# Kernel optimization log

Hardware: AMD Instinct MI355X
Metric: run time of the kernel (lower is better)

Reference implementation:

```python
import jax, jax.numpy as jnp
import numpy as np

D_MODEL = 512
NUM_HEADS = 8
D_FF = 2048
SEQ = 2048
BATCH = 2
EPS = 1e-5


def _linear(x, W, b):
    # x: [S,B,D_in], W: [D_out, D_in] (torch convention), b: [D_out]
    return jnp.einsum('sbd,ed->sbe', x, W) + b


def _layer_norm(x, g, b):
    mu = jnp.mean(x, axis=-1, keepdims=True)
    var = jnp.var(x, axis=-1, keepdims=True)
    return (x - mu) * jax.lax.rsqrt(var + EPS) * g + b


def _mha(q_in, k_in, v_in, W, b, mask4d, num_heads):
    # q_in: [Sq,B,D], k_in/v_in: [Sk,B,D]; W: [4,D,D], b: [4,D]
    Sq, B, D = q_in.shape
    Sk = k_in.shape[0]
    dk = D // num_heads
    q = _linear(q_in, W[0], b[0]).reshape(Sq, B, num_heads, dk).transpose(1, 2, 0, 3)
    k = _linear(k_in, W[1], b[1]).reshape(Sk, B, num_heads, dk).transpose(1, 2, 0, 3)
    v = _linear(v_in, W[2], b[2]).reshape(Sk, B, num_heads, dk).transpose(1, 2, 0, 3)
    scores = jnp.einsum('bhqd,bhkd->bhqk', q, k) / jnp.sqrt(jnp.asarray(dk, q.dtype))
    scores = jnp.where(mask4d, -jnp.inf, scores)
    p = jax.nn.softmax(scores, axis=-1)  # dropout p=0 -> identity
    o = jnp.einsum('bhqk,bhkd->bhqd', p, v)  # [B,H,Sq,dk]
    o = o.transpose(2, 0, 1, 3).reshape(Sq, B, D)
    return _linear(o, W[3], b[3])


def setup_inputs() -> dict:
    key = jax.random.key(0)
    ks = jax.random.split(key, 12)
    scale = 1.0 / np.sqrt(D_MODEL)
    inp = {
        'x': jax.random.normal(ks[0], (SEQ, BATCH, D_MODEL), jnp.float32),
        'memory': jax.random.normal(ks[1], (SEQ, BATCH, D_MODEL), jnp.float32),
        # causal mask: True = masked (strictly upper triangular)
        'tgt_mask': jnp.triu(jnp.ones((SEQ, SEQ), dtype=bool), k=1),
        # per-batch key padding mask for cross attention
        'memory_mask': jax.random.randint(ks[2], (BATCH, SEQ), 0, 2) > 0,
        'sa_W': jax.random.normal(ks[3], (4, D_MODEL, D_MODEL), jnp.float32) * scale,
        'sa_b': jnp.zeros((4, D_MODEL), jnp.float32),
        'ca_W': jax.random.normal(ks[4], (4, D_MODEL, D_MODEL), jnp.float32) * scale,
        'ca_b': jnp.zeros((4, D_MODEL), jnp.float32),
        'w1': jax.random.normal(ks[5], (D_FF, D_MODEL), jnp.float32) * scale,
        'b1': jnp.zeros((D_FF,), jnp.float32),
        'w2': jax.random.normal(ks[6], (D_MODEL, D_FF), jnp.float32) * (1.0 / np.sqrt(D_FF)),
        'b2': jnp.zeros((D_MODEL,), jnp.float32),
        'ln_g': jnp.ones((3, D_MODEL), jnp.float32),
        'ln_b': jnp.zeros((3, D_MODEL), jnp.float32),
    }
    return inp


def reference(x, memory, tgt_mask, memory_mask, sa_W, sa_b, ca_W, ca_b,
              w1, b1, w2, b2, ln_g, ln_b):
    # self-attention block (pre-norm, residual)
    nx = _layer_norm(x, ln_g[0], ln_b[0])
    sa = _mha(nx, nx, nx, sa_W, sa_b, tgt_mask[None, None], NUM_HEADS)
    x = x + sa
    # cross-attention block
    nx = _layer_norm(x, ln_g[1], ln_b[1])
    ca = _mha(nx, memory, memory, ca_W, ca_b, memory_mask[:, None, None, :], NUM_HEADS)
    x = x + ca
    # FFN block
    nx = _layer_norm(x, ln_g[2], ln_b[2])
    ff = _linear(jax.nn.relu(_linear(nx, w1, b1)), w2, b2)
    return x + ff
```

## Files before the change

### kernel.cpp

```cpp
#include <hip/hip_runtime.h>

#define S_LEN 2048
#define BATCH_N 2
#define DM 512
#define H_N 8
#define DK_N 64
#define FF_N 2048
#define M_TOK (S_LEN*BATCH_N)
#define QSZ (BATCH_N*H_N*S_LEN*DK_N)

typedef __attribute__((ext_vector_type(8))) short short8;
typedef __attribute__((ext_vector_type(4))) float f32x4;
typedef __attribute__((ext_vector_type(16))) float f32x16;
typedef __attribute__((ext_vector_type(4))) unsigned uint4v;

__device__ __forceinline__ unsigned short f2b(float f) {
  union { float f; unsigned u; } v; v.f = f;
  unsigned r = v.u + 0x7FFFu + ((v.u >> 16) & 1u);
  return (unsigned short)(r >> 16);
}
__device__ __forceinline__ float b2f(unsigned short u) {
  union { unsigned u; float f; } v; v.u = ((unsigned)u) << 16; return v.f;
}

__device__ __forceinline__ void gl_lds16(const void* g, void* l) {
  __builtin_amdgcn_global_load_lds(
      (__attribute__((address_space(1))) unsigned int*)(unsigned long long)g,
      (__attribute__((address_space(3))) unsigned int*)(unsigned int)(unsigned long long)l,
      16, 0, 0);
}

__global__ void cast_kernel(const float* __restrict__ src,
                            unsigned short* __restrict__ dst, int n) {
  int i = (blockIdx.x * blockDim.x + threadIdx.x) * 4;
  if (i >= n) return;
  float4 v = *(const float4*)(src + i);
  ushort4 o; o.x = f2b(v.x); o.y = f2b(v.y); o.z = f2b(v.z); o.w = f2b(v.w);
  *(ushort4*)(dst + i) = o;
}

__global__ void maskpack(const int* __restrict__ mm, unsigned long long* __restrict__ bm) {
  int t = threadIdx.x;
  int b = t >> 5, kt = t & 31;
  unsigned long long m = 0ull;
  for (int j = 0; j < 64; j++)
    m |= (unsigned long long)(mm[b*S_LEN + kt*64 + j] != 0) << j;
  bm[b*32 + kt] = m;
}

__global__ __launch_bounds__(128) void ln_kernel(const float* __restrict__ in,
                                                 const float* __restrict__ g,
                                                 const float* __restrict__ b,
                                                 unsigned short* __restrict__ out) {
  int row = blockIdx.x, t = threadIdx.x;
  float4 v = ((const float4*)(in + (size_t)row * DM))[t];
  float s  = v.x + v.y + v.z + v.w;
  float ss = v.x*v.x + v.y*v.y + v.z*v.z + v.w*v.w;
  #pragma unroll
  for (int off = 32; off >= 1; off >>= 1) {
    s  += __shfl_xor(s,  off);
    ss += __shfl_xor(ss, off);
  }
  __shared__ float sh[4];
  if ((t & 63) == 0) { sh[(t>>6)*2] = s; sh[(t>>6)*2+1] = ss; }
  __syncthreads();
  s = sh[0] + sh[2]; ss = sh[1] + sh[3];
  float mean = s * (1.f/512.f);
  float inv  = rsqrtf(ss * (1.f/512.f) - mean*mean + 1e-5f);
  float4 gv = ((const float4*)g)[t];
  float4 bv = ((const float4*)b)[t];
  ushort4 o;
  o.x = f2b((v.x-mean)*inv*gv.x + bv.x);
  o.y = f2b((v.y-mean)*inv*gv.y + bv.y);
  o.z = f2b((v.z-mean)*inv*gv.z + bv.z);
  o.w = f2b((v.w-mean)*inv*gv.w + bv.w);
  ((ushort4*)out)[(size_t)row*128 + t] = o;
}

template<int RELU, int OUTMODE, int RESID>
__global__ __launch_bounds__(256) void gemm_bt(
    const unsigned short* __restrict__ A, const unsigned short* __restrict__ W,
    const float* __restrict__ bias, const float* __restrict__ resid,
    float* __restrict__ Cf, unsigned short* __restrict__ Cb,
    int M, int N, int K)
{
  __shared__ unsigned short As[64*40];
  __shared__ unsigned short Bs[64*40];
  int tid = threadIdx.x;
  int lane = tid & 63, w = tid >> 6;
  int wr = w >> 1, wc = w & 1;
  int bm = blockIdx.y * 64, bn = blockIdx.x * 64;
  f32x4 acc[2][2] = {};
  int lrow = tid >> 2;
  int lcg  = (tid & 3) * 8;
  const size_t aoff = (size_t)(bm + lrow) * K + lcg;
  const size_t boff = (size_t)(bn + lrow) * K + lcg;
  int fr = lane & 15, kg = (lane >> 4) * 8;
  short8 pa = *(const short8*)&A[aoff];
  short8 pb = *(const short8*)&W[boff];
  for (int k0 = 0; k0 < K; k0 += 32) {
    *(short8*)&As[lrow*40 + lcg] = pa;
    *(short8*)&Bs[lrow*40 + lcg] = pb;
    if (k0 + 32 < K) {
      pa = *(const short8*)&A[aoff + k0 + 32];
      pb = *(const short8*)&W[boff + k0 + 32];
    }
    __syncthreads();
    short8 af0 = *(const short8*)&As[(wr*32 +      fr)*40 + kg];
    short8 af1 = *(const short8*)&As[(wr*32 + 16 + fr)*40 + kg];
    short8 bf0 = *(const short8*)&Bs[(wc*32 +      fr)*40 + kg];
    short8 bf1 = *(const short8*)&Bs[(wc*32 + 16 + fr)*40 + kg];
    acc[0][0] = __builtin_amdgcn_mfma_f32_16x16x32_bf16(af0, bf0, acc[0][0], 0,0,0);
    acc[0][1] = __builtin_amdgcn_mfma_f32_16x16x32_bf16(af0, bf1, acc[0][1], 0,0,0);
    acc[1][0] = __builtin_amdgcn_mfma_f32_16x16x32_bf16(af1, bf0, acc[1][0], 0,0,0);
    acc[1][1] = __builtin_amdgcn_mfma_f32_16x16x32_bf16(af1, bf1, acc[1][1], 0,0,0);
    __syncthreads();
  }
  int rbase = (lane >> 4) * 4;
  #pragma unroll
  for (int m = 0; m < 2; m++) {
    #pragma unroll
    for (int n = 0; n < 2; n++) {
      int col = bn + wc*32 + n*16 + (lane & 15);
      float bc = bias[col];
      #pragma unroll
      for (int r = 0; r < 4; r++) {
        int row = bm + wr*32 + m*16 + rbase + r;
        float vv = acc[m][n][r] + bc;
        if (RELU) vv = fmaxf(vv, 0.f);
        if (OUTMODE == 2) {
          int which = col >> 9, hh = (col >> 6) & 7, dd = col & 63;
          size_t idx = ((((size_t)which*BATCH_N + (row & 1))*H_N + hh)*S_LEN + (row >> 1))*DK_N + dd;
          Cb[idx] = f2b(vv);
        } else {
          size_t idx = (size_t)row * N + col;
          if (RESID) vv += resid[idx];
          if (OUTMODE == 1) Cb[idx] = f2b(vv);
          else              Cf[idx] = vv;
        }
      }
    }
  }
}

template<int RELU, int OUTMODE, int VSTART>
__global__ __launch_bounds__(256) void gemm128(
    const unsigned short* __restrict__ A, const unsigned short* __restrict__ W,
    const float* __restrict__ bias, unsigned short* __restrict__ Cb,
    int M, int N, int K)
{
  __shared__ unsigned short As[128*32];
  __shared__ unsigned short Bs[128*32];
  int tid = threadIdx.x, lane = tid & 63, w = tid >> 6;
  int bm = blockIdx.y * 128, bn = blockIdx.x * 128;
  int fr = lane & 15, hi = lane >> 4;
  int kg8 = hi*8, rg = hi*4;
  int wm = (w >> 1) * 64, wn = (w & 1) * 64;
  f32x4 acc[4][4] = {};
  const unsigned short* ga0 = A + (size_t)(bm +      (tid>>2))*K + (tid&3)*8;
  const unsigned short* ga1 = A + (size_t)(bm + 64 + (tid>>2))*K + (tid&3)*8;
  const unsigned short* gb0 = W + (size_t)(bn +      (tid>>2))*K + (tid&3)*8;
  const unsigned short* gb1 = W + (size_t)(bn + 64 + (tid>>2))*K + (tid&3)*8;
  unsigned short* lA0 = &As[tid*8];
  unsigned short* lA1 = &As[2048 + tid*8];
  unsigned short* lB0 = &Bs[tid*8];
  unsigned short* lB1 = &Bs[2048 + tid*8];
  for (int k0 = 0; k0 < K; k0 += 32) {
    gl_lds16(ga0 + k0, lA0);
    gl_lds16(ga1 + k0, lA1);
    gl_lds16(gb0 + k0, lB0);
    gl_lds16(gb1 + k0, lB1);
    __syncthreads();
    short8 af[4], bf[4];
    #pragma unroll
    for (int m = 0; m < 4; m++) af[m] = *(const short8*)&As[(wm + m*16 + fr)*32 + kg8];
    #pragma unroll
    for (int n = 0; n < 4; n++) bf[n] = *(const short8*)&Bs[(wn + n*16 + fr)*32 + kg8];
    __builtin_amdgcn_s_setprio(1);
    #pragma unroll
    for (int m = 0; m < 4; m++)
      #pragma unroll
      for (int n = 0; n < 4; n++)
        acc[m][n] = __builtin_amdgcn_mfma_f32_16x16x32_bf16(af[m], bf[n], acc[m][n], 0,0,0);
    __builtin_amdgcn_s_setprio(0);
    __syncthreads();
  }
  #pragma unroll
  for (int m = 0; m < 4; m++) {
    #pragma unroll
    for (int n = 0; n < 4; n++) {
      int col = bn + wn + n*16 + fr;
      float bc = bias[col];
      #pragma unroll
      for (int r = 0; r < 4; r++) {
        int row = bm + wm + m*16 + rg + r;
        float vv = acc[m][n][r] + bc;
        if (RELU) vv = fmaxf(vv, 0.f);
        if (OUTMODE == 2) {
          int which = col >> 9, hh = (col >> 6) & 7, dd = col & 63;
          int srow = row >> 1, bb = row & 1;
          size_t idx;
          if (which >= VSTART)
            idx = (size_t)which*QSZ + (((size_t)bb*H_N + hh)*DK_N + dd)*S_LEN + srow;
          else
            idx = (size_t)which*QSZ + (((size_t)bb*H_N + hh)*S_LEN + srow)*DK_N + dd;
          Cb[idx] = f2b(vv);
        } else {
          Cb[(size_t)row * N + col] = f2b(vv);
        }
      }
    }
  }
}

template<int MODE>
__global__ __launch_bounds__(256, 4) void attn2(
    const unsigned short* __restrict__ qg, const unsigned short* __restrict__ kpl,
    const unsigned short* __restrict__ vtpl, const unsigned long long* __restrict__ bm,
    unsigned short* __restrict__ opart, float* __restrict__ lpart)
{
  __shared__ unsigned short SM[2*64*72 + 128];
  unsigned short* Ks = SM;
  unsigned short* Vt = SM + 64*72;
  float* lsum = (float*)(SM + 2*64*72);
  int tid = threadIdx.x;
  int lane = tid & 63, w = tid >> 6;
  int qgp = w & 1, kh2 = w >> 1;
  int l31 = lane & 31, hi5 = lane >> 5;
  int bid = blockIdx.x;
  int p = bid & 15, u = bid >> 4;
  int qt = u >> 2, range = u & 3;
  int h = p & 7, b = p >> 3;
  const size_t sbase = (size_t)(b*H_N + h) * S_LEN;
  int kt0 = range*8, kt1 = kt0 + 7;
  if (MODE == 0) {
    if (kt0 > qt) {
      int zr = tid >> 2, zc = (tid & 3) * 16;
      short8 z = {};
      size_t zb = (size_t)range*QSZ + (sbase + (size_t)qt*64 + zr)*DK_N + zc;
      *(short8*)&opart[zb]     = z;
      *(short8*)&opart[zb + 8] = z;
      if (tid < 64) lpart[range*32768 + (int)sbase + qt*64 + tid] = 0.f;
      return;
    }
    if (kt1 > qt) kt1 = qt;
  }
  int qrow = qt*64 + qgp*32 + l31;
  short8 qf[4];
  #pragma unroll
  for (int km = 0; km < 4; km++)
    qf[km] = *(const short8*)&qg[(sbase + qrow)*DK_N + km*16 + hi5*8];

  f32x16 oa0 = {}, oa1 = {};
  float lp = 0.f;
  for (int kt = kt0; kt <= kt1; kt++) {
    __syncthreads();
    {
      int sr = tid >> 2, sc = (tid & 3) * 16;
      const unsigned short* kg = &kpl[(sbase + (size_t)kt*64 + sr)*DK_N + sc];
      *(short8*)&Ks[sr*72 + sc]     = *(const short8*)kg;
      *(short8*)&Ks[sr*72 + sc + 8] = *(const short8*)(kg + 8);
      const unsigned short* vg = &vtpl[((size_t)(b*H_N + h)*DK_N + sr)*S_LEN + kt*64 + sc];
      *(short8*)&Vt[sr*72 + sc]     = *(const short8*)vg;
      *(short8*)&Vt[sr*72 + sc + 8] = *(const short8*)(vg + 8);
    }
    __syncthreads();
    f32x16 sa = {};
    __builtin_amdgcn_s_setprio(1);
    #pragma unroll
    for (int km = 0; km < 4; km++) {
      short8 kf = *(const short8*)&Ks[(kh2*32 + l31)*72 + km*16 + hi5*8];
      sa = __builtin_amdgcn_mfma_f32_32x32x16_bf16(kf, qf[km], sa, 0, 0, 0);
    }
    __builtin_amdgcn_s_setprio(0);
    unsigned mlo = 0;
    if (MODE == 1) {
      unsigned long long mw = bm[b*32 + kt];
      mlo = (unsigned)(mw >> (kh2*32 + 4*hi5));
    }
    float pv[16];
    float psum = 0.f;
    int qv = qgp*32 + l31;
    #pragma unroll
    for (int r = 0; r < 16; r++) {
      const int pos = (r & 3) + 8*(r >> 2);
      float e = __expf(sa[r] * 0.125f);
      bool dead;
      if (MODE == 0) dead = (kt == qt) && (kh2*32 + 4*hi5 + pos > qv);
      else           dead = ((mlo >> pos) & 1u) != 0u;
      e = dead ? 0.f : e;
      pv[r] = e;
      psum += e;
    }
    lp += psum;
    unsigned pk[8];
    #pragma unroll
    for (int i = 0; i < 8; i++)
      asm("v_cvt_pk_bf16_f32 %0, %1, %2" : "=v"(pk[i]) : "v"(pv[2*i]), "v"(pv[2*i+1]));
    asm("v_permlane32_swap_b32 %0, %1" : "+v"(pk[0]), "+v"(pk[2]));
    asm("v_permlane32_swap_b32 %0, %1" : "+v"(pk[1]), "+v"(pk[3]));
    asm("v_permlane32_swap_b32 %0, %1" : "+v"(pk[4]), "+v"(pk[6]));
    asm("v_permlane32_swap_b32 %0, %1" : "+v"(pk[5]), "+v"(pk[7]));
    uint4v f0v, f1v;
    f0v.x = pk[0]; f0v.y = pk[1]; f0v.z = pk[2]; f0v.w = pk[3];
    f1v.x = pk[4]; f1v.y = pk[5]; f1v.z = pk[6]; f1v.w = pk[7];
    short8 pf0 = *(short8*)&f0v;
    short8 pf1 = *(short8*)&f1v;
    __builtin_amdgcn_s_setprio(1);
    {
      short8 v00 = *(const short8*)&Vt[(     l31)*72 + kh2*32 +      hi5*8];
      short8 v01 = *(const short8*)&Vt[(     l31)*72 + kh2*32 + 16 + hi5*8];
      oa0 = __builtin_amdgcn_mfma_f32_32x32x16_bf16(pf0, v00, oa0, 0, 0, 0);
      oa0 = __builtin_amdgcn_mfma_f32_32x32x16_bf16(pf1, v01, oa0, 0, 0, 0);
      short8 v10 = *(const short8*)&Vt[(32 + l31)*72 + kh2*32 +      hi5*8];
      short8 v11 = *(const short8*)&Vt[(32 + l31)*72 + kh2*32 + 16 + hi5*8];
      oa1 = __builtin_amdgcn_mfma_f32_32x32x16_bf16(pf0, v10, oa1, 0, 0, 0);
      oa1 = __builtin_amdgcn_mfma_f32_32x32x16_bf16(pf1, v11, oa1, 0, 0, 0);
    }
    __builtin_amdgcn_s_setprio(0);
  }
  float lptot = lp + __shfl_xor(lp, 32);
  float* fb = (float*)SM;
  __syncthreads();
  if (kh2 == 1) {
    #pragma unroll
    for (int r = 0; r < 16; r++) {
      const int pos = (r & 3) + 8*(r >> 2);
      int qr = qgp*32 + pos + 4*hi5;
      fb[qr*64 + l31]      = oa0[r];
      fb[qr*64 + 32 + l31] = oa1[r];
    }
    if (lane < 32) lsum[qgp*32 + l31] = lptot;
  }
  __syncthreads();
  if (kh2 == 0) {
    if (lane < 32)
      lpart[range*32768 + (int)sbase + qt*64 + qgp*32 + l31] = lptot + lsum[qgp*32 + l31];
    #pragma unroll
    for (int r = 0; r < 16; r++) {
      const int pos = (r & 3) + 8*(r >> 2);
      int qr = qgp*32 + pos + 4*hi5;
      size_t obase = (size_t)range*QSZ + (sbase + (size_t)qt*64 + qr)*DK_N;
      opart[obase + l31]      = f2b(oa0[r] + fb[qr*64 + l31]);
      opart[obase + 32 + l31] = f2b(oa1[r] + fb[qr*64 + 32 + l31]);
    }
  }
}

__global__ __launch_bounds__(256) void attn_combine4(
    const unsigned short* __restrict__ op, const float* __restrict__ lp,
    unsigned short* __restrict__ o)
{
  int t = blockIdx.x*256 + threadIdx.x;
  int f = t*8;
  int col = f & 511, row = f >> 9;
  int h = col >> 6, d = col & 63, s = row >> 1, b = row & 1;
  size_t pr = ((size_t)b*H_N + h)*S_LEN + s;
  size_t base = pr*DK_N + d;
  float acc[8] = {0.f,0.f,0.f,0.f,0.f,0.f,0.f,0.f};
  float l = 0.f;
  #pragma unroll
  for (int r = 0; r < 4; r++) {
    short8 a = *(const short8*)&op[(size_t)r*QSZ + base];
    #pragma unroll
    for (int i = 0; i < 8; i++) acc[i] += b2f((unsigned short)a[i]);
    l += lp[r*32768 + (int)pr];
  }
  float inv = 1.f / l;
  short8 r8;
  #pragma unroll
  for (int i = 0; i < 8; i++) r8[i] = (short)f2b(acc[i] * inv);
  *(short8*)&o[(size_t)row*DM + col] = r8;
}

extern "C" void kernel_launch(void* const* d_in, const int* in_sizes, int n_in,
                              void* d_out, int out_size, void* d_ws, size_t ws_size,
                              hipStream_t stream) {
  const float* x       = (const float*)d_in[0];
  const float* memory  = (const float*)d_in[1];
  const int*   memmask = (const int*)d_in[3];
  const float* sa_W = (const float*)d_in[4];
  const float* sa_b = (const float*)d_in[5];
  const float* ca_W = (const float*)d_in[6];
  const float* ca_b = (const float*)d_in[7];
  const float* w1   = (const float*)d_in[8];
  const float* b1   = (const float*)d_in[9];
  const float* w2   = (const float*)d_in[10];
  const float* b2   = (const float*)d_in[11];
  const float* ln_g = (const float*)d_in[12];
  const float* ln_b = (const float*)d_in[13];
  float* out = (float*)d_out;

  char* ws = (char*)d_ws;
  float*          xcur   = (float*)ws;
  unsigned short* nx_bf  = (unsigned short*)(ws + (8u<<20));
  unsigned short* qkv_sa = (unsigned short*)(ws + (12u<<20));
  unsigned short* q_ca   = (unsigned short*)(ws + (24u<<20));
  unsigned short* kv_ca  = (unsigned short*)(ws + (28u<<20));
  unsigned short* o_bf   = (unsigned short*)(ws + (36u<<20));
  unsigned short* mem_bf = (unsigned short*)(ws + (40u<<20));
  unsigned short* h_bf   = (unsigned short*)(ws + (44u<<20));
  unsigned short* opart  = (unsigned short*)(ws + (44u<<20));
  float*          lpart  = (float*)(ws + (60u<<20));
  unsigned long long* bmsk = (unsigned long long*)(ws + (60u<<20) + (1u<<19));
  unsigned short* w_sa   = (unsigned short*)(ws + (61u<<20));
  unsigned short* w_ca   = w_sa + 4*512*512;
  unsigned short* w_f1   = w_ca + 4*512*512;
  unsigned short* w_f2   = w_f1 + 2048*512;

  cast_kernel<<<1024, 256, 0, stream>>>(sa_W, w_sa, 4*512*512);
  cast_kernel<<<1024, 256, 0, stream>>>(ca_W, w_ca, 4*512*512);
  cast_kernel<<<1024, 256, 0, stream>>>(w1,   w_f1, 2048*512);
  cast_kernel<<<1024, 256, 0, stream>>>(w2,   w_f2, 512*2048);
  cast_kernel<<<2048, 256, 0, stream>>>(memory, mem_bf, M_TOK*512);
  maskpack<<<1, 64, 0, stream>>>(memmask, bmsk);

  dim3 blk(256);
  dim3 g512 (512/64,  4096/64);
  dim3 q128_1536(1536/128, 4096/128);
  dim3 q128_1024(1024/128, 4096/128);
  dim3 q128_2048(2048/128, 4096/128);

  ln_kernel<<<4096, 128, 0, stream>>>(x, ln_g, ln_b, nx_bf);
  gemm128<0,2,2><<<q128_1536, blk, 0, stream>>>(nx_bf, w_sa, sa_b, qkv_sa, 4096, 1536, 512);
  attn2<0><<<2048, 256, 0, stream>>>(qkv_sa, qkv_sa + QSZ, qkv_sa + 2*QSZ, nullptr, opart, lpart);
  attn_combine4<<<1024, 256, 0, stream>>>(opart, lpart, o_bf);
  gemm_bt<0,0,1><<<g512, blk, 0, stream>>>(o_bf, w_sa + 3*262144, sa_b + 1536, x, xcur, nullptr, 4096, 512, 512);

  ln_kernel<<<4096, 128, 0, stream>>>(xcur, ln_g + 512, ln_b + 512, nx_bf);
  gemm_bt<0,2,0><<<g512, blk, 0, stream>>>(nx_bf, w_ca, ca_b, nullptr, nullptr, q_ca, 4096, 512, 512);
  gemm128<0,2,1><<<q128_1024, blk, 0, stream>>>(mem_bf, w_ca + 262144, ca_b + 512, kv_ca, 4096, 1024, 512);
  attn2<1><<<2048, 256, 0, stream>>>(q_ca, kv_ca, kv_ca + QSZ, bmsk, opart, lpart);
  attn_combine4<<<1024, 256, 0, stream>>>(opart, lpart, o_bf);
  gemm_bt<0,0,1><<<g512, blk, 0, stream>>>(o_bf, w_ca + 3*262144, ca_b + 1536, xcur, xcur, nullptr, 4096, 512, 512);

  ln_kernel<<<4096, 128, 0, stream>>>(xcur, ln_g + 1024, ln_b + 1024, nx_bf);
  gemm128<1,1,0><<<q128_2048, blk, 0, stream>>>(nx_bf, w_f1, b1, h_bf, 4096, 2048, 512);
  gemm_bt<0,0,1><<<g512, blk, 0, stream>>>(h_bf, w_f2, b2, xcur, out, nullptr, 4096, 512, 2048);
}
```

Measured before the change: 212.3 us.

## Use 128-row query tiles in attention, double-buffer GEMM LDS, merge prep casts

The attention kernel now gives each wave its own 32 query rows over all 64 keys of a tile, with 128-query tiles per block. This halves the grid and drops the cross-wave LDS reduction of partial outputs, so each K/V tile loaded is reused by twice as many queries. The 64x64 GEMM gets double-buffered shared memory, which removes one barrier per k-step and overlaps the next tile's LDS store with the MFMAs. The six weight/memory cast and mask-pack launches are fused into a single prep kernel to cut launch overhead. In exchange, the attention kernel has a lower occupancy hint, fewer blocks and more causal imbalance per block.

```diff
diff --git a/kernel.cpp b/kernel.cpp
--- a/kernel.cpp
+++ b/kernel.cpp
@@ -30,22 +30,34 @@
       16, 0, 0);
 }
 
-__global__ void cast_kernel(const float* __restrict__ src,
-                            unsigned short* __restrict__ dst, int n) {
-  int i = (blockIdx.x * blockDim.x + threadIdx.x) * 4;
-  if (i >= n) return;
+__device__ __forceinline__ void cast4(const float* __restrict__ src,
+                                      unsigned short* __restrict__ dst, int i) {
   float4 v = *(const float4*)(src + i);
   ushort4 o; o.x = f2b(v.x); o.y = f2b(v.y); o.z = f2b(v.z); o.w = f2b(v.w);
   *(ushort4*)(dst + i) = o;
 }
 
-__global__ void maskpack(const int* __restrict__ mm, unsigned long long* __restrict__ bm) {
-  int t = threadIdx.x;
-  int b = t >> 5, kt = t & 31;
-  unsigned long long m = 0ull;
-  for (int j = 0; j < 64; j++)
-    m |= (unsigned long long)(mm[b*S_LEN + kt*64 + j] != 0) << j;
-  bm[b*32 + kt] = m;
+__global__ __launch_bounds__(256) void prep_kernel(
+    const float* __restrict__ sa_W, const float* __restrict__ ca_W,
+    const float* __restrict__ w1, const float* __restrict__ w2,
+    const float* __restrict__ memory, const int* __restrict__ mm,
+    unsigned short* __restrict__ o_sa, unsigned short* __restrict__ o_ca,
+    unsigned short* __restrict__ o_w1, unsigned short* __restrict__ o_w2,
+    unsigned short* __restrict__ o_mem, unsigned long long* __restrict__ bmo)
+{
+  int blk = blockIdx.x, t = threadIdx.x;
+  if (blk < 1024)      cast4(sa_W, o_sa, (blk*256 + t)*4);
+  else if (blk < 2048) cast4(ca_W, o_ca, ((blk-1024)*256 + t)*4);
+  else if (blk < 3072) cast4(w1,   o_w1, ((blk-2048)*256 + t)*4);
+  else if (blk < 4096) cast4(w2,   o_w2, ((blk-3072)*256 + t)*4);
+  else if (blk < 6144) cast4(memory, o_mem, ((blk-4096)*256 + t)*4);
+  else if (t < 64) {
+    int b = t >> 5, kt = t & 31;
+    unsigned long long m = 0ull;
+    for (int j = 0; j < 64; j++)
+      m |= (unsigned long long)(mm[b*S_LEN + kt*64 + j] != 0) << j;
+    bmo[b*32 + kt] = m;
+  }
 }
 
 __global__ __launch_bounds__(128) void ln_kernel(const float* __restrict__ in,
@@ -84,8 +96,8 @@
     float* __restrict__ Cf, unsigned short* __restrict__ Cb,
     int M, int N, int K)
 {
-  __shared__ unsigned short As[64*40];
-  __shared__ unsigned short Bs[64*40];
+  __shared__ unsigned short As[2][64*40];
+  __shared__ unsigned short Bs[2][64*40];
   int tid = threadIdx.x;
   int lane = tid & 63, w = tid >> 6;
   int wr = w >> 1, wc = w & 1;
@@ -98,23 +110,30 @@
   int fr = lane & 15, kg = (lane >> 4) * 8;
   short8 pa = *(const short8*)&A[aoff];
   short8 pb = *(const short8*)&W[boff];
+  *(short8*)&As[0][lrow*40 + lcg] = pa;
+  *(short8*)&Bs[0][lrow*40 + lcg] = pb;
+  __syncthreads();
+  int cur = 0;
   for (int k0 = 0; k0 < K; k0 += 32) {
-    *(short8*)&As[lrow*40 + lcg] = pa;
-    *(short8*)&Bs[lrow*40 + lcg] = pb;
-    if (k0 + 32 < K) {
+    bool hn = (k0 + 32) < K;
+    if (hn) {
       pa = *(const short8*)&A[aoff + k0 + 32];
       pb = *(const short8*)&W[boff + k0 + 32];
     }
-    __syncthreads();
-    short8 af0 = *(const short8*)&As[(wr*32 +      fr)*40 + kg];
-    short8 af1 = *(const short8*)&As[(wr*32 + 16 + fr)*40 + kg];
-    short8 bf0 = *(const short8*)&Bs[(wc*32 +      fr)*40 + kg];
-    short8 bf1 = *(const short8*)&Bs[(wc*32 + 16 + fr)*40 + kg];
+    short8 af0 = *(const short8*)&As[cur][(wr*32 +      fr)*40 + kg];
+    short8 af1 = *(const short8*)&As[cur][(wr*32 + 16 + fr)*40 + kg];
+    short8 bf0 = *(const short8*)&Bs[cur][(wc*32 +      fr)*40 + kg];
+    short8 bf1 = *(const short8*)&Bs[cur][(wc*32 + 16 + fr)*40 + kg];
     acc[0][0] = __builtin_amdgcn_mfma_f32_16x16x32_bf16(af0, bf0, acc[0][0], 0,0,0);
     acc[0][1] = __builtin_amdgcn_mfma_f32_16x16x32_bf16(af0, bf1, acc[0][1], 0,0,0);
     acc[1][0] = __builtin_amdgcn_mfma_f32_16x16x32_bf16(af1, bf0, acc[1][0], 0,0,0);
     acc[1][1] = __builtin_amdgcn_mfma_f32_16x16x32_bf16(af1, bf1, acc[1][1], 0,0,0);
+    if (hn) {
+      *(short8*)&As[cur^1][lrow*40 + lcg] = pa;
+      *(short8*)&Bs[cur^1][lrow*40 + lcg] = pb;
+    }
     __syncthreads();
+    cur ^= 1;
   }
   int rbase = (lane >> 4) * 4;
   #pragma unroll
@@ -214,136 +233,124 @@
 }
 
 template<int MODE>
-__global__ __launch_bounds__(256, 4) void attn2(
+__global__ __launch_bounds__(256, 3) void attn3(
     const unsigned short* __restrict__ qg, const unsigned short* __restrict__ kpl,
     const unsigned short* __restrict__ vtpl, const unsigned long long* __restrict__ bm,
     unsigned short* __restrict__ opart, float* __restrict__ lpart)
 {
-  __shared__ unsigned short SM[2*64*72 + 128];
+  __shared__ unsigned short SM[2*64*72];
   unsigned short* Ks = SM;
   unsigned short* Vt = SM + 64*72;
-  float* lsum = (float*)(SM + 2*64*72);
   int tid = threadIdx.x;
   int lane = tid & 63, w = tid >> 6;
-  int qgp = w & 1, kh2 = w >> 1;
   int l31 = lane & 31, hi5 = lane >> 5;
   int bid = blockIdx.x;
   int p = bid & 15, u = bid >> 4;
-  int qt = u >> 2, range = u & 3;
+  int qtile = u >> 2, range = u & 3;
   int h = p & 7, b = p >> 3;
   const size_t sbase = (size_t)(b*H_N + h) * S_LEN;
   int kt0 = range*8, kt1 = kt0 + 7;
   if (MODE == 0) {
-    if (kt0 > qt) {
-      int zr = tid >> 2, zc = (tid & 3) * 16;
+    int ktmax_tile = qtile*2 + 1;
+    if (kt0 > ktmax_tile) {
+      int zr = tid >> 1, zc = (tid & 1) * 32;
       short8 z = {};
-      size_t zb = (size_t)range*QSZ + (sbase + (size_t)qt*64 + zr)*DK_N + zc;
-      *(short8*)&opart[zb]     = z;
-      *(short8*)&opart[zb + 8] = z;
-      if (tid < 64) lpart[range*32768 + (int)sbase + qt*64 + tid] = 0.f;
+      size_t zb = (size_t)range*QSZ + (sbase + (size_t)qtile*128 + zr)*DK_N + zc;
+      *(short8*)&opart[zb]      = z;
+      *(short8*)&opart[zb + 8]  = z;
+      *(short8*)&opart[zb + 16] = z;
+      *(short8*)&opart[zb + 24] = z;
+      if (tid < 128) lpart[range*32768 + (int)sbase + qtile*128 + tid] = 0.f;
       return;
     }
-    if (kt1 > qt) kt1 = qt;
-  }
-  int qrow = qt*64 + qgp*32 + l31;
+    if (kt1 > ktmax_tile) kt1 = ktmax_tile;
+  }
+  int qrow = qtile*128 + w*32 + l31;
   short8 qf[4];
   #pragma unroll
   for (int km = 0; km < 4; km++)
     qf[km] = *(const short8*)&qg[(sbase + qrow)*DK_N + km*16 + hi5*8];
+
+  int sr = tid >> 2, sc = (tid & 3) * 16;
+  const unsigned short* kbase = &kpl[(sbase + sr)*DK_N + sc];
+  const unsigned short* vbase = &vtpl[((size_t)(b*H_N + h)*DK_N + sr)*S_LEN + sc];
 
   f32x16 oa0 = {}, oa1 = {};
   float lp = 0.f;
   for (int kt = kt0; kt <= kt1; kt++) {
     __syncthreads();
     {
-      int sr = tid >> 2, sc = (tid & 3) * 16;
-      const unsigned short* kg = &kpl[(sbase + (size_t)kt*64 + sr)*DK_N + sc];
+      const unsigned short* kg = kbase + (size_t)kt*64*DK_N;
+      const unsigned short* vg = vbase + kt*64;
       *(short8*)&Ks[sr*72 + sc]     = *(const short8*)kg;
       *(short8*)&Ks[sr*72 + sc + 8] = *(const short8*)(kg + 8);
-      const unsigned short* vg = &vtpl[((size_t)(b*H_N + h)*DK_N + sr)*S_LEN + kt*64 + sc];
       *(short8*)&Vt[sr*72 + sc]     = *(const short8*)vg;
       *(short8*)&Vt[sr*72 + sc + 8] = *(const short8*)(vg + 8);
     }
     __syncthreads();
-    f32x16 sa = {};
-    __builtin_amdgcn_s_setprio(1);
-    #pragma unroll
-    for (int km = 0; km < 4; km++) {
-      short8 kf = *(const short8*)&Ks[(kh2*32 + l31)*72 + km*16 + hi5*8];
-      sa = __builtin_amdgcn_mfma_f32_32x32x16_bf16(kf, qf[km], sa, 0, 0, 0);
-    }
-    __builtin_amdgcn_s_setprio(0);
-    unsigned mlo = 0;
-    if (MODE == 1) {
-      unsigned long long mw = bm[b*32 + kt];
-      mlo = (unsigned)(mw >> (kh2*32 + 4*hi5));
-    }
-    float pv[16];
-    float psum = 0.f;
-    int qv = qgp*32 + l31;
-    #pragma unroll
-    for (int r = 0; r < 16; r++) {
-      const int pos = (r & 3) + 8*(r >> 2);
-      float e = __expf(sa[r] * 0.125f);
-      bool dead;
-      if (MODE == 0) dead = (kt == qt) && (kh2*32 + 4*hi5 + pos > qv);
-      else           dead = ((mlo >> pos) & 1u) != 0u;
-      e = dead ? 0.f : e;
-      pv[r] = e;
-      psum += e;
-    }
-    lp += psum;
-    unsigned pk[8];
-    #pragma unroll
-    for (int i = 0; i < 8; i++)
-      asm("v_cvt_pk_bf16_f32 %0, %1, %2" : "=v"(pk[i]) : "v"(pv[2*i]), "v"(pv[2*i+1]));
-    asm("v_permlane32_swap_b32 %0, %1" : "+v"(pk[0]), "+v"(pk[2]));
-    asm("v_permlane32_swap_b32 %0, %1" : "+v"(pk[1]), "+v"(pk[3]));
-    asm("v_permlane32_swap_b32 %0, %1" : "+v"(pk[4]), "+v"(pk[6]));
-    asm("v_permlane32_swap_b32 %0, %1" : "+v"(pk[5]), "+v"(pk[7]));
-    uint4v f0v, f1v;
-    f0v.x = pk[0]; f0v.y = pk[1]; f0v.z = pk[2]; f0v.w = pk[3];
-    f1v.x = pk[4]; f1v.y = pk[5]; f1v.z = pk[6]; f1v.w = pk[7];
-    short8 pf0 = *(short8*)&f0v;
-    short8 pf1 = *(short8*)&f1v;
-    __builtin_amdgcn_s_setprio(1);
-    {
-      short8 v00 = *(const short8*)&Vt[(     l31)*72 + kh2*32 +      hi5*8];
-      short8 v01 = *(const short8*)&Vt[(     l31)*72 + kh2*32 + 16 + hi5*8];
-      oa0 = __builtin_amdgcn_mfma_f32_32x32x16_bf16(pf0, v00, oa0, 0, 0, 0);
-      oa0 = __builtin_amdgcn_mfma_f32_32x32x16_bf16(pf1, v01, oa0, 0, 0, 0);
-      short8 v10 = *(const short8*)&Vt[(32 + l31)*72 + kh2*32 +      hi5*8];
-      short8 v11 = *(const short8*)&Vt[(32 + l31)*72 + kh2*32 + 16 + hi5*8];
-      oa1 = __builtin_amdgcn_mfma_f32_32x32x16_bf16(pf0, v10, oa1, 0, 0, 0);
-      oa1 = __builtin_amdgcn_mfma_f32_32x32x16_bf16(pf1, v11, oa1, 0, 0, 0);
-    }
-    __builtin_amdgcn_s_setprio(0);
+    #pragma unroll
+    for (int kb = 0; kb < 2; kb++) {
+      f32x16 sa = {};
+      __builtin_amdgcn_s_setprio(1);
+      #pragma unroll
+      for (int km = 0; km < 4; km++) {
+        short8 kf = *(const short8*)&Ks[(kb*32 + l31)*72 + km*16 + hi5*8];
+        sa = __builtin_amdgcn_mfma_f32_32x32x16_bf16(kf, qf[km], sa, 0, 0, 0);
+      }
+      __builtin_amdgcn_s_setprio(0);
+      unsigned mlo = 0;
+      if (MODE == 1) mlo = (unsigned)(bm[b*32 + kt] >> (kb*32 + 4*hi5));
+      float pv[16];
+      float psum = 0.f;
+      #pragma unroll
+      for (int r = 0; r < 16; r++) {
+        const int pos = (r & 3) + 8*(r >> 2);
+        float e = __expf(sa[r] * 0.125f);
+        bool dead;
+        if (MODE == 0) dead = (kt*64 + kb*32 + 4*hi5 + pos) > qrow;
+        else           dead = ((mlo >> pos) & 1u) != 0u;
+        e = dead ? 0.f : e;
+        pv[r] = e;
+        psum += e;
+      }
+      lp += psum;
+      unsigned pk[8];
+      #pragma unroll
+      for (int i = 0; i < 8; i++)
+        asm("v_cvt_pk_bf16_f32 %0, %1, %2" : "=v"(pk[i]) : "v"(pv[2*i]), "v"(pv[2*i+1]));
+      asm("v_permlane32_swap_b32 %0, %1" : "+v"(pk[0]), "+v"(pk[2]));
+      asm("v_permlane32_swap_b32 %0, %1" : "+v"(pk[1]), "+v"(pk[3]));
+      asm("v_permlane32_swap_b32 %0, %1" : "+v"(pk[4]), "+v"(pk[6]));
+      asm("v_permlane32_swap_b32 %0, %1" : "+v"(pk[5]), "+v"(pk[7]));
+      uint4v f0v, f1v;
+      f0v.x = pk[0]; f0v.y = pk[1]; f0v.z = pk[2]; f0v.w = pk[3];
+      f1v.x = pk[4]; f1v.y = pk[5]; f1v.z = pk[6]; f1v.w = pk[7];
+      short8 pf0 = *(short8*)&f0v;
+      short8 pf1 = *(short8*)&f1v;
+      __builtin_amdgcn_s_setprio(1);
+      {
+        short8 v00 = *(const short8*)&Vt[(     l31)*72 + kb*32 +      hi5*8];
+        short8 v01 = *(const short8*)&Vt[(     l31)*72 + kb*32 + 16 + hi5*8];
+        oa0 = __builtin_amdgcn_mfma_f32_32x32x16_bf16(pf0, v00, oa0, 0, 0, 0);
+        oa0 = __builtin_amdgcn_mfma_f32_32x32x16_bf16(pf1, v01, oa0, 0, 0, 0);
+        short8 v10 = *(const short8*)&Vt[(32 + l31)*72 + kb*32 +      hi5*8];
+        short8 v11 = *(const short8*)&Vt[(32 + l31)*72 + kb*32 + 16 + hi5*8];
+        oa1 = __builtin_amdgcn_mfma_f32_32x32x16_bf16(pf0, v10, oa1, 0, 0, 0);
+        oa1 = __builtin_amdgcn_mfma_f32_32x32x16_bf16(pf1, v11, oa1, 0, 0, 0);
+      }
+      __builtin_amdgcn_s_setprio(0);
+    }
   }
   float lptot = lp + __shfl_xor(lp, 32);
-  float* fb = (float*)SM;
-  __syncthreads();
-  if (kh2 == 1) {
-    #pragma unroll
-    for (int r = 0; r < 16; r++) {
-      const int pos = (r & 3) + 8*(r >> 2);
-      int qr = qgp*32 + pos + 4*hi5;
-      fb[qr*64 + l31]      = oa0[r];
-      fb[qr*64 + 32 + l31] = oa1[r];
-    }
-    if (lane < 32) lsum[qgp*32 + l31] = lptot;
-  }
-  __syncthreads();
-  if (kh2 == 0) {
-    if (lane < 32)
-      lpart[range*32768 + (int)sbase + qt*64 + qgp*32 + l31] = lptot + lsum[qgp*32 + l31];
-    #pragma unroll
-    for (int r = 0; r < 16; r++) {
-      const int pos = (r & 3) + 8*(r >> 2);
-      int qr = qgp*32 + pos + 4*hi5;
-      size_t obase = (size_t)range*QSZ + (sbase + (size_t)qt*64 + qr)*DK_N;
-      opart[obase + l31]      = f2b(oa0[r] + fb[qr*64 + l31]);
-      opart[obase + 32 + l31] = f2b(oa1[r] + fb[qr*64 + 32 + l31]);
-    }
+  if (lane < 32)
+    lpart[range*32768 + (int)sbase + qtile*128 + w*32 + l31] = lptot;
+  #pragma unroll
+  for (int r = 0; r < 16; r++) {
+    const int pos = (r & 3) + 8*(r >> 2);
+    int qr = qtile*128 + w*32 + pos + 4*hi5;
+    size_t obase = (size_t)range*QSZ + (sbase + (size_t)qr)*DK_N;
+    opart[obase + l31]      = f2b(oa0[r]);
+    opart[obase + 32 + l31] = f2b(oa1[r]);
   }
 }
 
@@ -408,12 +415,8 @@
   unsigned short* w_f1   = w_ca + 4*512*512;
   unsigned short* w_f2   = w_f1 + 2048*512;
 
-  cast_kernel<<<1024, 256, 0, stream>>>(sa_W, w_sa, 4*512*512);
-  cast_kernel<<<1024, 256, 0, stream>>>(ca_W, w_ca, 4*512*512);
-  cast_kernel<<<1024, 256, 0, stream>>>(w1,   w_f1, 2048*512);
-  cast_kernel<<<1024, 256, 0, stream>>>(w2,   w_f2, 512*2048);
-  cast_kernel<<<2048, 256, 0, stream>>>(memory, mem_bf, M_TOK*512);
-  maskpack<<<1, 64, 0, stream>>>(memmask, bmsk);
+  prep_kernel<<<6145, 256, 0, stream>>>(sa_W, ca_W, w1, w2, memory, memmask,
+                                        w_sa, w_ca, w_f1, w_f2, mem_bf, bmsk);
 
   dim3 blk(256);
   dim3 g512 (512/64,  4096/64);
@@ -423,14 +426,14 @@
 
   ln_kernel<<<4096, 128, 0, stream>>>(x, ln_g, ln_b, nx_bf);
   gemm128<0,2,2><<<q128_1536, blk, 0, stream>>>(nx_bf, w_sa, sa_b, qkv_sa, 4096, 1536, 512);
-  attn2<0><<<2048, 256, 0, stream>>>(qkv_sa, qkv_sa + QSZ, qkv_sa + 2*QSZ, nullptr, opart, lpart);
+  attn3<0><<<1024, 256, 0, stream>>>(qkv_sa, qkv_sa + QSZ, qkv_sa + 2*QSZ, nullptr, opart, lpart);
   attn_combine4<<<1024, 256, 0, stream>>>(opart, lpart, o_bf);
   gemm_bt<0,0,1><<<g512, blk, 0, stream>>>(o_bf, w_sa + 3*262144, sa_b + 1536, x, xcur, nullptr, 4096, 512, 512);
 
   ln_kernel<<<4096, 128, 0, stream>>>(xcur, ln_g + 512, ln_b + 512, nx_bf);
   gemm_bt<0,2,0><<<g512, blk, 0, stream>>>(nx_bf, w_ca, ca_b, nullptr, nullptr, q_ca, 4096, 512, 512);
   gemm128<0,2,1><<<q128_1024, blk, 0, stream>>>(mem_bf, w_ca + 262144, ca_b + 512, kv_ca, 4096, 1024, 512);
-  attn2<1><<<2048, 256, 0, stream>>>(q_ca, kv_ca, kv_ca + QSZ, bmsk, opart, lpart);
+  attn3<1><<<1024, 256, 0, stream>>>(q_ca, kv_ca, kv_ca + QSZ, bmsk, opart, lpart);
   attn_combine4<<<1024, 256, 0, stream>>>(opart, lpart, o_bf);
   gemm_bt<0,0,1><<<g512, blk, 0, stream>>>(o_bf, w_ca + 3*262144, ca_b + 1536, xcur, xcur, nullptr, 4096, 512, 512);
 
```

Result: no change. 208.7 us (-1.7%).
